# Performance work log

Measured on AMD Instinct MI355X. Metric: run time of the kernel, lower is better.

Reference implementation:

```python
import jax, jax.numpy as jnp
import numpy as np

B, F, V, E = 16384, 20, 100000, 32
D_BOT = F * E            # 640
DIMS = (512, 256)        # bottom MLP dims
TDIMS = (128, 64)        # tower hidden dims
N_DOM = 4


def setup_inputs() -> dict:
    key = jax.random.key(0)
    ks = jax.random.split(key, 16)
    inp = {
        "feature_ids": jax.random.randint(ks[0], (B, F), 0, V, dtype=jnp.int64),
        "domain_id": jax.random.randint(ks[1], (B,), 0, N_DOM, dtype=jnp.int64),
        # embedding tables [F, V, E]
        "emb": jax.random.normal(ks[2], (F, V, E), dtype=jnp.float32) * 0.01,
        # bottom MLP: 640 -> 512 -> 256 (relu, no output layer)
        "W1": jax.random.normal(ks[3], (D_BOT, DIMS[0]), dtype=jnp.float32) * (1.0 / np.sqrt(D_BOT)),
        "b1": jnp.zeros((DIMS[0],), dtype=jnp.float32),
        "W2": jax.random.normal(ks[4], (DIMS[0], DIMS[1]), dtype=jnp.float32) * (1.0 / np.sqrt(DIMS[0])),
        "b2": jnp.zeros((DIMS[1],), dtype=jnp.float32),
        # towers (stacked over domain dim): 256 -> 128 -> 64 -> 1
        "TW1": jax.random.normal(ks[5], (N_DOM, DIMS[1], TDIMS[0]), dtype=jnp.float32) * (1.0 / np.sqrt(DIMS[1])),
        "Tb1": jnp.zeros((N_DOM, TDIMS[0]), dtype=jnp.float32),
        "TW2": jax.random.normal(ks[6], (N_DOM, TDIMS[0], TDIMS[1]), dtype=jnp.float32) * (1.0 / np.sqrt(TDIMS[0])),
        "Tb2": jnp.zeros((N_DOM, TDIMS[1]), dtype=jnp.float32),
        "TW3": jax.random.normal(ks[7], (N_DOM, TDIMS[1], 1), dtype=jnp.float32) * (1.0 / np.sqrt(TDIMS[1])),
        "Tb3": jnp.zeros((N_DOM, 1), dtype=jnp.float32),
    }
    return inp


def reference(feature_ids, domain_id, emb, W1, b1, W2, b2, TW1, Tb1, TW2, Tb2, TW3, Tb3):
    # Embedding lookup + concat: [B, F, E] -> [B, F*E]
    e = emb[jnp.arange(F)[None, :], feature_ids]          # [B, F, E]
    h = e.reshape(B, F * E)
    # Shared bottom MLP (relu)
    h = jax.nn.relu(h @ W1 + b1)                          # [B, 512]
    h = jax.nn.relu(h @ W2 + b2)                          # [B, 256]
    # All domain towers computed densely for every sample (faithful to source)
    t = jax.nn.relu(jnp.einsum('bi,dio->bdo', h, TW1) + Tb1[None])   # [B, D, 128]
    t = jax.nn.relu(jnp.einsum('bdi,dio->bdo', t, TW2) + Tb2[None])  # [B, D, 64]
    logit = jnp.einsum('bdi,dio->bdo', t, TW3) + Tb3[None]           # [B, D, 1]
    ys = jax.nn.sigmoid(logit)[..., 0]                    # [B, D]
    # Select per-sample domain output via mask (domains are exclusive)
    onehot = jax.nn.one_hot(domain_id, N_DOM, dtype=ys.dtype)        # [B, D]
    final = jnp.sum(ys * onehot, axis=1)                  # [B]
    return final
```

## Files before the change

### kernel.cpp

```cpp
#include <hip/hip_runtime.h>

#define B_SZ  16384
#define F_SZ  20
#define V_SZ  100000
#define E_SZ  32
#define DBOT  640
#define D1    512
#define D2    256
#define T1D   128
#define T2D   64
#define NDOM  4

typedef __bf16 bf16x8 __attribute__((ext_vector_type(8)));
typedef float  f32x4  __attribute__((ext_vector_type(4)));

#define MFMA(a, b, c) __builtin_amdgcn_mfma_f32_16x16x32_bf16((a), (b), (c), 0, 0, 0)

__global__ __launch_bounds__(256) void k_prep(const float* __restrict__ W1,
                                              const float* __restrict__ W2,
                                              const float* __restrict__ TW1,
                                              const float* __restrict__ TW2,
                                              __bf16* __restrict__ W1P,
                                              __bf16* __restrict__ W2P,
                                              __bf16* __restrict__ TW1P,
                                              __bf16* __restrict__ TW2P) {
  int bid = blockIdx.x, tid = threadIdx.x;
  const float* src; __bf16* dst; int n, k, N;
  if (bid < 160) {
    long g = (long)bid * 256 + tid;
    int lane = g & 63; int kkg = (int)((g >> 6) % 20); int ntile = (int)(g / 1280);
    n = ntile * 16 + (lane & 15); k = kkg * 32 + ((lane >> 4) << 3);
    src = W1; N = D1; dst = W1P + g * 8;
  } else if (bid < 224) {
    long g = (long)(bid - 160) * 256 + tid;
    int lane = g & 63; int kkg = (int)((g >> 6) & 15); int ntile = (int)(g >> 10);
    n = ntile * 16 + (lane & 15); k = kkg * 32 + ((lane >> 4) << 3);
    src = W2; N = D2; dst = W2P + g * 8;
  } else if (bid < 288) {
    long g = (long)(bid - 224) * 256 + tid;
    int d = (int)(g >> 12); long r = g & 4095;
    int lane = r & 63; int kkg = (int)((r >> 6) & 7); int ntile = (int)(r >> 9);
    n = ntile * 16 + (lane & 15); k = kkg * 32 + ((lane >> 4) << 3);
    src = TW1 + (long)d * D2 * T1D; N = T1D;
    dst = TW1P + ((long)(d * 64 + ntile * 8 + kkg) * 64 + lane) * 8;
  } else {
    long g = (long)(bid - 288) * 256 + tid;
    int d = (int)(g >> 10); long r = g & 1023;
    int lane = r & 63; int kkg = (int)((r >> 6) & 3); int ntile = (int)(r >> 8);
    n = ntile * 16 + (lane & 15); k = kkg * 32 + ((lane >> 4) << 3);
    src = TW2 + (long)d * T1D * T2D; N = T2D;
    dst = TW2P + ((long)(d * 16 + ntile * 4 + kkg) * 64 + lane) * 8;
  }
  bf16x8 o;
#pragma unroll
  for (int e = 0; e < 8; ++e) o[e] = (__bf16)src[(long)(k + e) * N + n];
  *(bf16x8*)dst = o;
}

__global__ __launch_bounds__(512) void k_mega(const int* __restrict__ fids,
                                              const int* __restrict__ dom,
                                              const float* __restrict__ emb,
                                              const __bf16* __restrict__ W1P,
                                              const float* __restrict__ b1,
                                              const __bf16* __restrict__ W2P,
                                              const float* __restrict__ b2,
                                              const __bf16* __restrict__ TW1P,
                                              const __bf16* __restrict__ TW2P,
                                              const float* __restrict__ Tb1,
                                              const float* __restrict__ Tb2,
                                              const float* __restrict__ TW3,
                                              const float* __restrict__ Tb3,
                                              float* __restrict__ out) {
  __shared__ __attribute__((aligned(16))) char smem[152576];
  int*    ids_lds = (int*)(smem + 147456);
  __bf16* sA      = (__bf16*)smem;
  __bf16* h1      = (__bf16*)(smem + 81920);
  __bf16* h2_lds  = (__bf16*)smem;
  __bf16* t_lds   = (__bf16*)(smem + 32768);

  int bid = blockIdx.x, tid = threadIdx.x;
  int lane = tid & 63, w = tid >> 6;
  int lrow = lane & 15, kq = lane >> 4;
  int m0 = bid * 64;

  for (int i = tid; i < 64 * F_SZ; i += 512) ids_lds[i] = fids[m0 * F_SZ + i];
  __syncthreads();

  {
    float4 ga[10], gb[10];
    int sb[10];
#pragma unroll
    for (int i = 0; i < 10; ++i) {
      unsigned c = tid + i * 512;
      unsigned row = c / 80;
      unsigned cc = c - row * 80;
      int f = cc >> 2, es = (cc & 3) << 3;
      int id = ids_lds[row * F_SZ + f];
      const float* p = emb + ((long)f * V_SZ + id) * E_SZ + es;
      ga[i] = *(const float4*)p;
      gb[i] = *(const float4*)(p + 4);
      sb[i] = (int)(row * 1280 + cc * 16) ^ ((row & 7) << 4);
    }
#pragma unroll
    for (int i = 0; i < 10; ++i) {
      bf16x8 o;
      o[0] = (__bf16)ga[i].x; o[1] = (__bf16)ga[i].y;
      o[2] = (__bf16)ga[i].z; o[3] = (__bf16)ga[i].w;
      o[4] = (__bf16)gb[i].x; o[5] = (__bf16)gb[i].y;
      o[6] = (__bf16)gb[i].z; o[7] = (__bf16)gb[i].w;
      *(bf16x8*)((char*)sA + sb[i]) = o;
    }
  }
  __syncthreads();

  {
    f32x4 acc[4][4] = {};
#pragma unroll
    for (int f = 0; f < F_SZ; ++f) {
      bf16x8 af[4];
#pragma unroll
      for (int mi = 0; mi < 4; ++mi) {
        int byte = ((mi * 16 + lrow) * 1280 + (f * 32 + kq * 8) * 2) ^ ((lrow & 7) << 4);
        af[mi] = *(const bf16x8*)((const char*)sA + byte);
      }
#pragma unroll
      for (int ni = 0; ni < 4; ++ni) {
        bf16x8 bfr = *(const bf16x8*)(W1P +
            ((long)((w * 4 + ni) * 20 + f) * 64 + lane) * 8);
#pragma unroll
        for (int mi = 0; mi < 4; ++mi)
          acc[mi][ni] = MFMA(af[mi], bfr, acc[mi][ni]);
      }
    }
#pragma unroll
    for (int ni = 0; ni < 4; ++ni) {
      int col = w * 64 + ni * 16 + lrow;
      float bv = b1[col];
#pragma unroll
      for (int mi = 0; mi < 4; ++mi) {
#pragma unroll
        for (int r = 0; r < 4; ++r) {
          int row = mi * 16 + kq * 4 + r;
          float v = acc[mi][ni][r] + bv;
          v = v > 0.f ? v : 0.f;
          int byte = (row * 1024 + col * 2) ^ ((row & 7) << 4);
          *(__bf16*)((char*)h1 + byte) = (__bf16)v;
        }
      }
    }
  }
  __syncthreads();

  {
    f32x4 acc2[4][2] = {};
#pragma unroll 4
    for (int kkg = 0; kkg < 16; ++kkg) {
      bf16x8 a2[4];
#pragma unroll
      for (int mi = 0; mi < 4; ++mi) {
        int byte = ((mi * 16 + lrow) * 1024 + kkg * 64 + kq * 16) ^ ((lrow & 7) << 4);
        a2[mi] = *(const bf16x8*)((const char*)h1 + byte);
      }
#pragma unroll
      for (int ni = 0; ni < 2; ++ni) {
        bf16x8 bfr = *(const bf16x8*)(W2P +
            ((long)((w * 2 + ni) * 16 + kkg) * 64 + lane) * 8);
#pragma unroll
        for (int mi = 0; mi < 4; ++mi)
          acc2[mi][ni] = MFMA(a2[mi], bfr, acc2[mi][ni]);
      }
    }
#pragma unroll
    for (int ni = 0; ni < 2; ++ni) {
      int col = w * 32 + ni * 16 + lrow;
      float bv = b2[col];
#pragma unroll
      for (int mi = 0; mi < 4; ++mi) {
#pragma unroll
        for (int r = 0; r < 4; ++r) {
          int row = mi * 16 + kq * 4 + r;
          float v = acc2[mi][ni][r] + bv;
          v = v > 0.f ? v : 0.f;
          int byte = (row * 512 + col * 2) ^ ((row & 7) << 4);
          *(__bf16*)((char*)h2_lds + byte) = (__bf16)v;
        }
      }
    }
  }
  __syncthreads();

  {
    int r0 = (w & 3) * 16;
    int d0 = (w >> 2) * 2;
    int grow = r0 + lrow;
    int mydom = dom[m0 + grow];
    __bf16* tw = t_lds + w * 2048;

    bf16x8 a1[8];
#pragma unroll
    for (int kk = 0; kk < 8; ++kk) {
      int byte = (grow * 512 + (kk * 32 + kq * 8) * 2) ^ ((grow & 7) << 4);
      a1[kk] = *(const bf16x8*)((const char*)h2_lds + byte);
    }

#pragma unroll
    for (int dd = 0; dd < 2; ++dd) {
      int d = d0 + dd;
      f32x4 acc1[8] = {};
#pragma unroll
      for (int kk = 0; kk < 8; ++kk) {
#pragma unroll
        for (int ni = 0; ni < 8; ++ni) {
          bf16x8 b = *(const bf16x8*)(TW1P +
              ((long)(d * 64 + ni * 8 + kk) * 64 + lane) * 8);
          acc1[ni] = MFMA(a1[kk], b, acc1[ni]);
        }
      }
#pragma unroll
      for (int ni = 0; ni < 8; ++ni) {
        float bv = Tb1[d * T1D + ni * 16 + lrow];
#pragma unroll
        for (int r = 0; r < 4; ++r) {
          float v = acc1[ni][r] + bv;
          v = v > 0.f ? v : 0.f;
          tw[(kq * 4 + r) * 128 + ni * 16 + lrow] = (__bf16)v;
        }
      }
      asm volatile("s_waitcnt lgkmcnt(0)" ::: "memory");

      bf16x8 a2f[4];
#pragma unroll
      for (int kk = 0; kk < 4; ++kk)
        a2f[kk] = *(const bf16x8*)(&tw[lrow * 128 + kk * 32 + kq * 8]);
      f32x4 acc2[4] = {};
#pragma unroll
      for (int kk = 0; kk < 4; ++kk) {
#pragma unroll
        for (int ni = 0; ni < 4; ++ni) {
          bf16x8 b = *(const bf16x8*)(TW2P +
              ((long)(d * 16 + ni * 4 + kk) * 64 + lane) * 8);
          acc2[ni] = MFMA(a2f[kk], b, acc2[ni]);
        }
      }
      asm volatile("s_waitcnt lgkmcnt(0)" ::: "memory");
#pragma unroll
      for (int ni = 0; ni < 4; ++ni) {
        float bv = Tb2[d * T2D + ni * 16 + lrow];
#pragma unroll
        for (int r = 0; r < 4; ++r) {
          float v = acc2[ni][r] + bv;
          v = v > 0.f ? v : 0.f;
          tw[(kq * 4 + r) * 64 + ni * 16 + lrow] = (__bf16)v;
        }
      }
      asm volatile("s_waitcnt lgkmcnt(0)" ::: "memory");

      float s = 0.f;
#pragma unroll
      for (int j = 0; j < 16; ++j)
        s += (float)tw[lrow * 64 + kq * 16 + j] * TW3[d * T2D + kq * 16 + j];
      s += __shfl_xor(s, 16);
      s += __shfl_xor(s, 32);
      s += Tb3[d];
      if (kq == 0 && mydom == d)
        out[m0 + grow] = 1.0f / (1.0f + expf(-s));
      asm volatile("s_waitcnt lgkmcnt(0)" ::: "memory");
    }
  }
}

extern "C" void kernel_launch(void* const* d_in, const int* in_sizes, int n_in,
                              void* d_out, int out_size, void* d_ws, size_t ws_size,
                              hipStream_t stream) {
  const int*   fids = (const int*)d_in[0];
  const int*   dom  = (const int*)d_in[1];
  const float* emb  = (const float*)d_in[2];
  const float* W1   = (const float*)d_in[3];
  const float* b1   = (const float*)d_in[4];
  const float* W2   = (const float*)d_in[5];
  const float* b2   = (const float*)d_in[6];
  const float* TW1  = (const float*)d_in[7];
  const float* Tb1  = (const float*)d_in[8];
  const float* TW2  = (const float*)d_in[9];
  const float* Tb2  = (const float*)d_in[10];
  const float* TW3  = (const float*)d_in[11];
  const float* Tb3  = (const float*)d_in[12];
  float* out = (float*)d_out;

  char* ws = (char*)d_ws;
  __bf16* W1P   = (__bf16*)(ws);
  __bf16* W2P   = (__bf16*)(ws + 655360);
  __bf16* TW1P  = (__bf16*)(ws + 917504);
  __bf16* TW2P  = (__bf16*)(ws + 1179648);

  k_prep<<<304, 256, 0, stream>>>(W1, W2, TW1, TW2, W1P, W2P, TW1P, TW2P);
  k_mega<<<256, 512, 0, stream>>>(fids, dom, emb, W1P, b1, W2P, b2,
                                  TW1P, TW2P, Tb1, Tb2, TW3, Tb3, out);
}
```

Measured before the change: 50.03 us.

## Assign one domain per wave pair in tower stage to reuse weight fragments

The tower stage now gives each wave a single domain and 32 rows (two 16-row M tiles) instead of 16 rows across two domains. Each TW1/TW2 fragment loaded from global memory feeds two MFMAs, halving weight traffic per block and removing the serial per-domain loop. The intermediate tower buffers move to a larger LDS region with XOR swizzling to avoid bank conflicts. The cost is more accumulator registers per wave, which could reduce occupancy or cause spills.

```diff
diff --git a/kernel.cpp b/kernel.cpp
--- a/kernel.cpp
+++ b/kernel.cpp
@@ -76,7 +76,7 @@
   __bf16* sA      = (__bf16*)smem;
   __bf16* h1      = (__bf16*)(smem + 81920);
   __bf16* h2_lds  = (__bf16*)smem;
-  __bf16* t_lds   = (__bf16*)(smem + 32768);
+  __bf16* t_lds   = (__bf16*)(smem + 81920);
 
   int bid = blockIdx.x, tid = threadIdx.x;
   int lane = tid & 63, w = tid >> 6;
@@ -190,81 +190,103 @@
   __syncthreads();
 
   {
-    int r0 = (w & 3) * 16;
-    int d0 = (w >> 2) * 2;
-    int grow = r0 + lrow;
-    int mydom = dom[m0 + grow];
-    __bf16* tw = t_lds + w * 2048;
-
-    bf16x8 a1[8];
+    int d  = w >> 1;
+    int r0 = (w & 1) * 32;
+    __bf16* tw = t_lds + w * 4096;
+
+    bf16x8 a1[2][8];
+#pragma unroll
+    for (int mi = 0; mi < 2; ++mi)
+#pragma unroll
+      for (int kk = 0; kk < 8; ++kk) {
+        int row = r0 + mi * 16 + lrow;
+        int byte = (row * 512 + (kk * 32 + kq * 8) * 2) ^ ((row & 7) << 4);
+        a1[mi][kk] = *(const bf16x8*)((const char*)h2_lds + byte);
+      }
+
+    f32x4 acc1[2][8] = {};
 #pragma unroll
     for (int kk = 0; kk < 8; ++kk) {
-      int byte = (grow * 512 + (kk * 32 + kq * 8) * 2) ^ ((grow & 7) << 4);
-      a1[kk] = *(const bf16x8*)((const char*)h2_lds + byte);
-    }
-
-#pragma unroll
-    for (int dd = 0; dd < 2; ++dd) {
-      int d = d0 + dd;
-      f32x4 acc1[8] = {};
-#pragma unroll
-      for (int kk = 0; kk < 8; ++kk) {
-#pragma unroll
-        for (int ni = 0; ni < 8; ++ni) {
-          bf16x8 b = *(const bf16x8*)(TW1P +
-              ((long)(d * 64 + ni * 8 + kk) * 64 + lane) * 8);
-          acc1[ni] = MFMA(a1[kk], b, acc1[ni]);
+#pragma unroll
+      for (int ni = 0; ni < 8; ++ni) {
+        bf16x8 b = *(const bf16x8*)(TW1P +
+            ((long)(d * 64 + ni * 8 + kk) * 64 + lane) * 8);
+#pragma unroll
+        for (int mi = 0; mi < 2; ++mi)
+          acc1[mi][ni] = MFMA(a1[mi][kk], b, acc1[mi][ni]);
+      }
+    }
+#pragma unroll
+    for (int ni = 0; ni < 8; ++ni) {
+      float bv = Tb1[d * T1D + ni * 16 + lrow];
+#pragma unroll
+      for (int mi = 0; mi < 2; ++mi) {
+#pragma unroll
+        for (int r = 0; r < 4; ++r) {
+          int lr = mi * 16 + kq * 4 + r;
+          float v = acc1[mi][ni][r] + bv;
+          v = v > 0.f ? v : 0.f;
+          int byte = (lr * 256 + (ni * 16 + lrow) * 2) ^ ((lr & 7) << 4);
+          *(__bf16*)((char*)tw + byte) = (__bf16)v;
         }
       }
-#pragma unroll
-      for (int ni = 0; ni < 8; ++ni) {
-        float bv = Tb1[d * T1D + ni * 16 + lrow];
+    }
+    asm volatile("s_waitcnt lgkmcnt(0)" ::: "memory");
+
+    bf16x8 a2f[2][4];
+#pragma unroll
+    for (int mi = 0; mi < 2; ++mi)
+#pragma unroll
+      for (int kk = 0; kk < 4; ++kk) {
+        int lr = mi * 16 + lrow;
+        int byte = (lr * 256 + (kk * 32 + kq * 8) * 2) ^ ((lr & 7) << 4);
+        a2f[mi][kk] = *(const bf16x8*)((const char*)tw + byte);
+      }
+    asm volatile("s_waitcnt lgkmcnt(0)" ::: "memory");
+    f32x4 acc2[2][4] = {};
+#pragma unroll
+    for (int kk = 0; kk < 4; ++kk) {
+#pragma unroll
+      for (int ni = 0; ni < 4; ++ni) {
+        bf16x8 b = *(const bf16x8*)(TW2P +
+            ((long)(d * 16 + ni * 4 + kk) * 64 + lane) * 8);
+#pragma unroll
+        for (int mi = 0; mi < 2; ++mi)
+          acc2[mi][ni] = MFMA(a2f[mi][kk], b, acc2[mi][ni]);
+      }
+    }
+#pragma unroll
+    for (int ni = 0; ni < 4; ++ni) {
+      float bv = Tb2[d * T2D + ni * 16 + lrow];
+#pragma unroll
+      for (int mi = 0; mi < 2; ++mi) {
 #pragma unroll
         for (int r = 0; r < 4; ++r) {
-          float v = acc1[ni][r] + bv;
+          int lr = mi * 16 + kq * 4 + r;
+          float v = acc2[mi][ni][r] + bv;
           v = v > 0.f ? v : 0.f;
-          tw[(kq * 4 + r) * 128 + ni * 16 + lrow] = (__bf16)v;
+          int byte = (lr * 128 + (ni * 16 + lrow) * 2) ^ ((lr & 7) << 4);
+          *(__bf16*)((char*)tw + byte) = (__bf16)v;
         }
       }
-      asm volatile("s_waitcnt lgkmcnt(0)" ::: "memory");
-
-      bf16x8 a2f[4];
-#pragma unroll
-      for (int kk = 0; kk < 4; ++kk)
-        a2f[kk] = *(const bf16x8*)(&tw[lrow * 128 + kk * 32 + kq * 8]);
-      f32x4 acc2[4] = {};
-#pragma unroll
-      for (int kk = 0; kk < 4; ++kk) {
-#pragma unroll
-        for (int ni = 0; ni < 4; ++ni) {
-          bf16x8 b = *(const bf16x8*)(TW2P +
-              ((long)(d * 16 + ni * 4 + kk) * 64 + lane) * 8);
-          acc2[ni] = MFMA(a2f[kk], b, acc2[ni]);
-        }
-      }
-      asm volatile("s_waitcnt lgkmcnt(0)" ::: "memory");
-#pragma unroll
-      for (int ni = 0; ni < 4; ++ni) {
-        float bv = Tb2[d * T2D + ni * 16 + lrow];
-#pragma unroll
-        for (int r = 0; r < 4; ++r) {
-          float v = acc2[ni][r] + bv;
-          v = v > 0.f ? v : 0.f;
-          tw[(kq * 4 + r) * 64 + ni * 16 + lrow] = (__bf16)v;
-        }
-      }
-      asm volatile("s_waitcnt lgkmcnt(0)" ::: "memory");
-
+    }
+    asm volatile("s_waitcnt lgkmcnt(0)" ::: "memory");
+
+    {
+      int lr    = (kq & 1) * 16 + lrow;
+      int khalf = kq >> 1;
       float s = 0.f;
 #pragma unroll
-      for (int j = 0; j < 16; ++j)
-        s += (float)tw[lrow * 64 + kq * 16 + j] * TW3[d * T2D + kq * 16 + j];
-      s += __shfl_xor(s, 16);
+      for (int j = 0; j < 32; ++j) {
+        int col = khalf * 32 + j;
+        int byte = (lr * 128 + col * 2) ^ ((lr & 7) << 4);
+        s += (float)*(const __bf16*)((const char*)tw + byte) * TW3[d * T2D + col];
+      }
       s += __shfl_xor(s, 32);
       s += Tb3[d];
-      if (kq == 0 && mydom == d)
+      int grow = r0 + lr;
+      if (khalf == 0 && dom[m0 + grow] == d)
         out[m0 + grow] = 1.0f / (1.0f + expf(-s));
-      asm volatile("s_waitcnt lgkmcnt(0)" ::: "memory");
     }
   }
 }
```

Result: faster. 47.10 us (-5.9%).

## Double block to 1024 threads and pipeline embedding gather with layer-1 MFMA

Applied to the files above, without the earlier changes.

The block grows from 8 to 16 waves, so each wave now computes half as many output columns per GEMM and a single tower domain instead of two. The embedding gather is split into five feature groups, and the next group's global loads are issued while the current group's MFMAs run. Tower scratch moves to a separate LDS region with XOR swizzling to reduce bank conflicts. This buys more latency hiding and parallelism per CU, at the cost of extra barriers per group and higher register pressure under the 1024-thread launch bound.

```diff
diff --git a/kernel.cpp b/kernel.cpp
--- a/kernel.cpp
+++ b/kernel.cpp
@@ -57,66 +57,81 @@
   *(bf16x8*)dst = o;
 }
 
-__global__ __launch_bounds__(512) void k_mega(const int* __restrict__ fids,
-                                              const int* __restrict__ dom,
-                                              const float* __restrict__ emb,
-                                              const __bf16* __restrict__ W1P,
-                                              const float* __restrict__ b1,
-                                              const __bf16* __restrict__ W2P,
-                                              const float* __restrict__ b2,
-                                              const __bf16* __restrict__ TW1P,
-                                              const __bf16* __restrict__ TW2P,
-                                              const float* __restrict__ Tb1,
-                                              const float* __restrict__ Tb2,
-                                              const float* __restrict__ TW3,
-                                              const float* __restrict__ Tb3,
-                                              float* __restrict__ out) {
+__global__ __launch_bounds__(1024) void k_mega(const int* __restrict__ fids,
+                                               const int* __restrict__ dom,
+                                               const float* __restrict__ emb,
+                                               const __bf16* __restrict__ W1P,
+                                               const float* __restrict__ b1,
+                                               const __bf16* __restrict__ W2P,
+                                               const float* __restrict__ b2,
+                                               const __bf16* __restrict__ TW1P,
+                                               const __bf16* __restrict__ TW2P,
+                                               const float* __restrict__ Tb1,
+                                               const float* __restrict__ Tb2,
+                                               const float* __restrict__ TW3,
+                                               const float* __restrict__ Tb3,
+                                               float* __restrict__ out) {
   __shared__ __attribute__((aligned(16))) char smem[152576];
   int*    ids_lds = (int*)(smem + 147456);
   __bf16* sA      = (__bf16*)smem;
   __bf16* h1      = (__bf16*)(smem + 81920);
   __bf16* h2_lds  = (__bf16*)smem;
-  __bf16* t_lds   = (__bf16*)(smem + 32768);
+  __bf16* t_lds   = (__bf16*)(smem + 81920);
 
   int bid = blockIdx.x, tid = threadIdx.x;
   int lane = tid & 63, w = tid >> 6;
   int lrow = lane & 15, kq = lane >> 4;
   int m0 = bid * 64;
 
-  for (int i = tid; i < 64 * F_SZ; i += 512) ids_lds[i] = fids[m0 * F_SZ + i];
+  for (int i = tid; i < 64 * F_SZ; i += 1024) ids_lds[i] = fids[m0 * F_SZ + i];
   __syncthreads();
 
+  int grow0 = tid >> 4, cc = tid & 15;
+  int sb0 = (grow0 * 1280 + cc * 16) ^ ((grow0 & 7) << 4);
+  int fbase = cc >> 2, es = (cc & 3) << 3;
+
+  float4 g0a, g0b;
   {
-    float4 ga[10], gb[10];
-    int sb[10];
-#pragma unroll
-    for (int i = 0; i < 10; ++i) {
-      unsigned c = tid + i * 512;
-      unsigned row = c / 80;
-      unsigned cc = c - row * 80;
-      int f = cc >> 2, es = (cc & 3) << 3;
-      int id = ids_lds[row * F_SZ + f];
+    int f = fbase;
+    int id = ids_lds[grow0 * F_SZ + f];
+    const float* p = emb + ((long)f * V_SZ + id) * E_SZ + es;
+    g0a = *(const float4*)p; g0b = *(const float4*)(p + 4);
+  }
+
+  f32x4 acc[4][2] = {};
+
+#pragma unroll
+  for (int g = 0; g < 5; ++g) {
+    {
+      bf16x8 o;
+      o[0] = (__bf16)g0a.x; o[1] = (__bf16)g0a.y; o[2] = (__bf16)g0a.z; o[3] = (__bf16)g0a.w;
+      o[4] = (__bf16)g0b.x; o[5] = (__bf16)g0b.y; o[6] = (__bf16)g0b.z; o[7] = (__bf16)g0b.w;
+      *(bf16x8*)((char*)sA + sb0 + g * 256) = o;
+    }
+    asm volatile("s_waitcnt lgkmcnt(0)" ::: "memory");
+    __builtin_amdgcn_s_barrier();
+    __builtin_amdgcn_sched_barrier(0);
+
+    bf16x8 bfr[4][2];
+#pragma unroll
+    for (int f4 = 0; f4 < 4; ++f4)
+#pragma unroll
+      for (int ni = 0; ni < 2; ++ni)
+        bfr[f4][ni] = *(const bf16x8*)(W1P +
+            ((long)((w * 2 + ni) * 20 + g * 4 + f4) * 64 + lane) * 8);
+    __builtin_amdgcn_sched_barrier(0);
+
+    if (g < 4) {
+      int f = (g + 1) * 4 + fbase;
+      int id = ids_lds[grow0 * F_SZ + f];
       const float* p = emb + ((long)f * V_SZ + id) * E_SZ + es;
-      ga[i] = *(const float4*)p;
-      gb[i] = *(const float4*)(p + 4);
-      sb[i] = (int)(row * 1280 + cc * 16) ^ ((row & 7) << 4);
-    }
-#pragma unroll
-    for (int i = 0; i < 10; ++i) {
-      bf16x8 o;
-      o[0] = (__bf16)ga[i].x; o[1] = (__bf16)ga[i].y;
-      o[2] = (__bf16)ga[i].z; o[3] = (__bf16)ga[i].w;
-      o[4] = (__bf16)gb[i].x; o[5] = (__bf16)gb[i].y;
-      o[6] = (__bf16)gb[i].z; o[7] = (__bf16)gb[i].w;
-      *(bf16x8*)((char*)sA + sb[i]) = o;
-    }
-  }
-  __syncthreads();
-
-  {
-    f32x4 acc[4][4] = {};
-#pragma unroll
-    for (int f = 0; f < F_SZ; ++f) {
+      g0a = *(const float4*)p; g0b = *(const float4*)(p + 4);
+    }
+    __builtin_amdgcn_sched_barrier(0);
+
+#pragma unroll
+    for (int f4 = 0; f4 < 4; ++f4) {
+      int f = g * 4 + f4;
       bf16x8 af[4];
 #pragma unroll
       for (int mi = 0; mi < 4; ++mi) {
@@ -124,35 +139,33 @@
         af[mi] = *(const bf16x8*)((const char*)sA + byte);
       }
 #pragma unroll
-      for (int ni = 0; ni < 4; ++ni) {
-        bf16x8 bfr = *(const bf16x8*)(W1P +
-            ((long)((w * 4 + ni) * 20 + f) * 64 + lane) * 8);
+      for (int ni = 0; ni < 2; ++ni)
 #pragma unroll
         for (int mi = 0; mi < 4; ++mi)
-          acc[mi][ni] = MFMA(af[mi], bfr, acc[mi][ni]);
-      }
-    }
-#pragma unroll
-    for (int ni = 0; ni < 4; ++ni) {
-      int col = w * 64 + ni * 16 + lrow;
-      float bv = b1[col];
-#pragma unroll
-      for (int mi = 0; mi < 4; ++mi) {
-#pragma unroll
-        for (int r = 0; r < 4; ++r) {
-          int row = mi * 16 + kq * 4 + r;
-          float v = acc[mi][ni][r] + bv;
-          v = v > 0.f ? v : 0.f;
-          int byte = (row * 1024 + col * 2) ^ ((row & 7) << 4);
-          *(__bf16*)((char*)h1 + byte) = (__bf16)v;
-        }
+          acc[mi][ni] = MFMA(af[mi], bfr[f4][ni], acc[mi][ni]);
+    }
+  }
+
+#pragma unroll
+  for (int ni = 0; ni < 2; ++ni) {
+    int col = w * 32 + ni * 16 + lrow;
+    float bv = b1[col];
+#pragma unroll
+    for (int mi = 0; mi < 4; ++mi) {
+#pragma unroll
+      for (int r = 0; r < 4; ++r) {
+        int row = mi * 16 + kq * 4 + r;
+        float v = acc[mi][ni][r] + bv;
+        v = v > 0.f ? v : 0.f;
+        int byte = (row * 1024 + col * 2) ^ ((row & 7) << 4);
+        *(__bf16*)((char*)h1 + byte) = (__bf16)v;
       }
     }
   }
   __syncthreads();
 
   {
-    f32x4 acc2[4][2] = {};
+    f32x4 acc2[4] = {};
 #pragma unroll 4
     for (int kkg = 0; kkg < 16; ++kkg) {
       bf16x8 a2[4];
@@ -161,25 +174,21 @@
         int byte = ((mi * 16 + lrow) * 1024 + kkg * 64 + kq * 16) ^ ((lrow & 7) << 4);
         a2[mi] = *(const bf16x8*)((const char*)h1 + byte);
       }
-#pragma unroll
-      for (int ni = 0; ni < 2; ++ni) {
-        bf16x8 bfr = *(const bf16x8*)(W2P +
-            ((long)((w * 2 + ni) * 16 + kkg) * 64 + lane) * 8);
-#pragma unroll
-        for (int mi = 0; mi < 4; ++mi)
-          acc2[mi][ni] = MFMA(a2[mi], bfr, acc2[mi][ni]);
-      }
-    }
-#pragma unroll
-    for (int ni = 0; ni < 2; ++ni) {
-      int col = w * 32 + ni * 16 + lrow;
+      bf16x8 bfr2 = *(const bf16x8*)(W2P +
+          ((long)(w * 16 + kkg) * 64 + lane) * 8);
+#pragma unroll
+      for (int mi = 0; mi < 4; ++mi)
+        acc2[mi] = MFMA(a2[mi], bfr2, acc2[mi]);
+    }
+    {
+      int col = w * 16 + lrow;
       float bv = b2[col];
 #pragma unroll
       for (int mi = 0; mi < 4; ++mi) {
 #pragma unroll
         for (int r = 0; r < 4; ++r) {
           int row = mi * 16 + kq * 4 + r;
-          float v = acc2[mi][ni][r] + bv;
+          float v = acc2[mi][r] + bv;
           v = v > 0.f ? v : 0.f;
           int byte = (row * 512 + col * 2) ^ ((row & 7) << 4);
           *(__bf16*)((char*)h2_lds + byte) = (__bf16)v;
@@ -190,81 +199,87 @@
   __syncthreads();
 
   {
+    int d  = w >> 2;
     int r0 = (w & 3) * 16;
-    int d0 = (w >> 2) * 2;
-    int grow = r0 + lrow;
-    int mydom = dom[m0 + grow];
     __bf16* tw = t_lds + w * 2048;
 
     bf16x8 a1[8];
 #pragma unroll
     for (int kk = 0; kk < 8; ++kk) {
-      int byte = (grow * 512 + (kk * 32 + kq * 8) * 2) ^ ((grow & 7) << 4);
+      int row = r0 + lrow;
+      int byte = (row * 512 + (kk * 32 + kq * 8) * 2) ^ ((row & 7) << 4);
       a1[kk] = *(const bf16x8*)((const char*)h2_lds + byte);
     }
 
-#pragma unroll
-    for (int dd = 0; dd < 2; ++dd) {
-      int d = d0 + dd;
-      f32x4 acc1[8] = {};
-#pragma unroll
-      for (int kk = 0; kk < 8; ++kk) {
-#pragma unroll
-        for (int ni = 0; ni < 8; ++ni) {
-          bf16x8 b = *(const bf16x8*)(TW1P +
-              ((long)(d * 64 + ni * 8 + kk) * 64 + lane) * 8);
-          acc1[ni] = MFMA(a1[kk], b, acc1[ni]);
-        }
-      }
+    f32x4 acc1[8] = {};
+#pragma unroll
+    for (int kk = 0; kk < 8; ++kk) {
 #pragma unroll
       for (int ni = 0; ni < 8; ++ni) {
-        float bv = Tb1[d * T1D + ni * 16 + lrow];
-#pragma unroll
-        for (int r = 0; r < 4; ++r) {
-          float v = acc1[ni][r] + bv;
-          v = v > 0.f ? v : 0.f;
-          tw[(kq * 4 + r) * 128 + ni * 16 + lrow] = (__bf16)v;
-        }
-      }
-      asm volatile("s_waitcnt lgkmcnt(0)" ::: "memory");
-
-      bf16x8 a2f[4];
-#pragma unroll
-      for (int kk = 0; kk < 4; ++kk)
-        a2f[kk] = *(const bf16x8*)(&tw[lrow * 128 + kk * 32 + kq * 8]);
-      f32x4 acc2[4] = {};
-#pragma unroll
-      for (int kk = 0; kk < 4; ++kk) {
-#pragma unroll
-        for (int ni = 0; ni < 4; ++ni) {
-          bf16x8 b = *(const bf16x8*)(TW2P +
-              ((long)(d * 16 + ni * 4 + kk) * 64 + lane) * 8);
-          acc2[ni] = MFMA(a2f[kk], b, acc2[ni]);
-        }
-      }
-      asm volatile("s_waitcnt lgkmcnt(0)" ::: "memory");
+        bf16x8 b = *(const bf16x8*)(TW1P +
+            ((long)(d * 64 + ni * 8 + kk) * 64 + lane) * 8);
+        acc1[ni] = MFMA(a1[kk], b, acc1[ni]);
+      }
+    }
+#pragma unroll
+    for (int ni = 0; ni < 8; ++ni) {
+      float bv = Tb1[d * T1D + ni * 16 + lrow];
+#pragma unroll
+      for (int r = 0; r < 4; ++r) {
+        int lr = kq * 4 + r;
+        float v = acc1[ni][r] + bv;
+        v = v > 0.f ? v : 0.f;
+        int byte = (lr * 256 + (ni * 16 + lrow) * 2) ^ ((lr & 7) << 4);
+        *(__bf16*)((char*)tw + byte) = (__bf16)v;
+      }
+    }
+    asm volatile("s_waitcnt lgkmcnt(0)" ::: "memory");
+
+    bf16x8 a2f[4];
+#pragma unroll
+    for (int kk = 0; kk < 4; ++kk) {
+      int byte = (lrow * 256 + (kk * 32 + kq * 8) * 2) ^ ((lrow & 7) << 4);
+      a2f[kk] = *(const bf16x8*)((const char*)tw + byte);
+    }
+    asm volatile("s_waitcnt lgkmcnt(0)" ::: "memory");
+    f32x4 acc2[4] = {};
+#pragma unroll
+    for (int kk = 0; kk < 4; ++kk) {
 #pragma unroll
       for (int ni = 0; ni < 4; ++ni) {
-        float bv = Tb2[d * T2D + ni * 16 + lrow];
-#pragma unroll
-        for (int r = 0; r < 4; ++r) {
-          float v = acc2[ni][r] + bv;
-          v = v > 0.f ? v : 0.f;
-          tw[(kq * 4 + r) * 64 + ni * 16 + lrow] = (__bf16)v;
-        }
-      }
-      asm volatile("s_waitcnt lgkmcnt(0)" ::: "memory");
-
+        bf16x8 b = *(const bf16x8*)(TW2P +
+            ((long)(d * 16 + ni * 4 + kk) * 64 + lane) * 8);
+        acc2[ni] = MFMA(a2f[kk], b, acc2[ni]);
+      }
+    }
+#pragma unroll
+    for (int ni = 0; ni < 4; ++ni) {
+      float bv = Tb2[d * T2D + ni * 16 + lrow];
+#pragma unroll
+      for (int r = 0; r < 4; ++r) {
+        int lr = kq * 4 + r;
+        float v = acc2[ni][r] + bv;
+        v = v > 0.f ? v : 0.f;
+        int byte = (lr * 128 + (ni * 16 + lrow) * 2) ^ ((lr & 7) << 4);
+        *(__bf16*)((char*)tw + byte) = (__bf16)v;
+      }
+    }
+    asm volatile("s_waitcnt lgkmcnt(0)" ::: "memory");
+
+    {
       float s = 0.f;
 #pragma unroll
-      for (int j = 0; j < 16; ++j)
-        s += (float)tw[lrow * 64 + kq * 16 + j] * TW3[d * T2D + kq * 16 + j];
+      for (int j = 0; j < 16; ++j) {
+        int col = kq * 16 + j;
+        int byte = (lrow * 128 + col * 2) ^ ((lrow & 7) << 4);
+        s += (float)*(const __bf16*)((const char*)tw + byte) * TW3[d * T2D + col];
+      }
       s += __shfl_xor(s, 16);
       s += __shfl_xor(s, 32);
       s += Tb3[d];
-      if (kq == 0 && mydom == d)
+      int grow = r0 + lrow;
+      if (kq == 0 && dom[m0 + grow] == d)
         out[m0 + grow] = 1.0f / (1.0f + expf(-s));
-      asm volatile("s_waitcnt lgkmcnt(0)" ::: "memory");
     }
   }
 }
@@ -294,6 +309,6 @@
   __bf16* TW2P  = (__bf16*)(ws + 1179648);
 
   k_prep<<<304, 256, 0, stream>>>(W1, W2, TW1, TW2, W1P, W2P, TW1P, TW2P);
-  k_mega<<<256, 512, 0, stream>>>(fids, dom, emb, W1P, b1, W2P, b2,
-                                  TW1P, TW2P, Tb1, Tb2, TW3, Tb3, out);
+  k_mega<<<256, 1024, 0, stream>>>(fids, dom, emb, W1P, b1, W2P, b2,
+                                   TW1P, TW2P, Tb1, Tb2, TW3, Tb3, out);
 }
```

Measured after the change: 52.06 us. 1.04x slower.
